# Optimization experiments

Hardware: AMD Instinct MI355X
Metric: run time of the kernel (lower is better)

Reference implementation:

```python
import jax, jax.numpy as jnp
import numpy as np
from jax import lax

R_NOBOUNDARY, R_BOUNDARY, SMALL_M, BIG_M = 5, 20, 3, 6
NUM_CLASSES, EMBED = 20, 2048


def _conv1d(x, w, pad):
    # x: [B, Cin, T], w: [Cout, Cin, K] -> [B, Cout, T]
    return lax.conv_general_dilated(x, w, (1,), [(pad, pad)],
                                    dimension_numbers=('NCH', 'OIH', 'NCH'))


def _erode(b, k):
    # scipy binary_erosion with structure ones((1,k)), border_value=0:
    # out[i] = min over window [i - k//2, i + k-1 - k//2], zero-padded
    c = k // 2
    xp = jnp.pad(b, ((0, 0), (c, k - 1 - c)))
    return lax.reduce_window(xp, jnp.inf, lax.min, (1, k), (1, 1), 'VALID')


def _dilate(b, k):
    # scipy binary_dilation reflects the structure: window [i-(k-1-c), i+c]
    c = k // 2
    xp = jnp.pad(b, ((0, 0), (k - 1 - c, c)))
    return lax.reduce_window(xp, -jnp.inf, lax.max, (1, k), (1, 1), 'VALID')


def _select_topk(scores, emb, k):
    # scores: [B,T], emb: [B,T,D] -> ([B,k,D], [B,k])
    _, idx = lax.top_k(scores, k)
    sel = jnp.take_along_axis(emb, idx[:, :, None], axis=1)
    return sel, idx


def setup_inputs() -> dict:
    key = jax.random.key(0)
    ks = jax.random.split(key, 6)
    B, T = 16, 750
    x = jax.random.normal(ks[0], (B, T, 2048), dtype=jnp.float32)
    s_embed = 1.0 / np.sqrt(1024 * 3)
    w_rgb = jax.random.normal(ks[1], (EMBED, 1024, 3), dtype=jnp.float32) * s_embed
    b_rgb = jnp.zeros((EMBED,), dtype=jnp.float32)
    w_flow = jax.random.normal(ks[2], (EMBED, 1024, 3), dtype=jnp.float32) * s_embed
    b_flow = jnp.zeros((EMBED,), dtype=jnp.float32)
    w_cls = jax.random.normal(ks[3], (NUM_CLASSES, EMBED, 1), dtype=jnp.float32) / np.sqrt(EMBED)
    return {'x': x, 'w_rgb': w_rgb, 'b_rgb': b_rgb, 'w_flow': w_flow,
            'b_flow': b_flow, 'w_cls': w_cls}


def reference(x, w_rgb, b_rgb, w_flow, b_flow, w_cls):
    # Dropout layers are identity (eval mode).
    T = x.shape[1]
    k_nb = T // R_NOBOUNDARY
    k_b = T // R_BOUNDARY

    rgb = jnp.transpose(x[:, :, 0:1024], (0, 2, 1))    # [B,1024,T]
    flow = jnp.transpose(x[:, :, 1024:2048], (0, 2, 1))
    out = (jax.nn.relu(_conv1d(rgb, w_rgb, 1) + b_rgb[None, :, None])
           + jax.nn.relu(_conv1d(flow, w_flow, 1) + b_flow[None, :, None]))  # [B,2048,T]
    embeddings = jnp.transpose(out, (0, 2, 1))          # [B,T,2048]
    cas = jnp.transpose(jax.nn.relu(_conv1d(out, w_cls, 0)), (0, 2, 1))  # [B,T,C]
    actionness = cas.sum(axis=2)                        # [B,T]

    # no-boundary mining (dropout identity in eval)
    act_rev = jnp.max(actionness, axis=1, keepdims=True) - actionness
    EA, idx = _select_topk(actionness, embeddings, k_nb)
    EB, _ = _select_topk(act_rev, embeddings, k_nb)

    # boundary mining via 1D morphology on binarized actionness
    med = jnp.median(actionness, axis=1, keepdims=True)
    aness_bin = (actionness > med).astype(actionness.dtype)  # [B,T]
    inner = _erode(aness_bin, SMALL_M) - _erode(aness_bin, BIG_M)
    HA, _ = _select_topk(actionness * inner, embeddings, k_b)
    outer = _dilate(aness_bin, BIG_M) - _dilate(aness_bin, SMALL_M)
    HB, _ = _select_topk(actionness * outer, embeddings, k_b)

    # video-level class scores: per-class top-k mean over time, softmax over classes
    cas_ct = jnp.transpose(cas, (0, 2, 1))              # [B,C,T]
    topk_scores, _ = lax.top_k(cas_ct, k_nb)            # [B,C,k_nb]
    video_scores = jax.nn.softmax(topk_scores.mean(axis=2), axis=1)  # [B,C]

    return (video_scores, EA, EB, HA, HB, idx, actionness, cas, embeddings)
```

## Files before the change

### kernel.cpp

```cpp
#include <hip/hip_runtime.h>
#include <stdint.h>
#include <math.h>

#define B_   16
#define T_   750
#define NC_  20
#define KNB_ 150
#define KB_  37

typedef _Float16 f16x8 __attribute__((ext_vector_type(8)));
typedef _Float16 f16x4 __attribute__((ext_vector_type(4)));
typedef float    f32x4 __attribute__((ext_vector_type(4)));

static constexpr long long O_VS  = 0;
static constexpr long long O_EA  = 320;
static constexpr long long O_EB  = 320 + 4915200LL;
static constexpr long long O_HA  = 320 + 2*4915200LL;
static constexpr long long O_HB  = O_HA + 1212416LL;
static constexpr long long O_IDX = O_HB + 1212416LL;
static constexpr long long O_ACT = O_IDX + 2400LL;
static constexpr long long O_CAS = O_ACT + 12000LL;
static constexpr long long O_EMB = O_CAS + 240000LL;

static constexpr long long WX_ELE   = 16LL * 752 * 2048;
static constexpr long long W_XHI    = 0;
static constexpr long long W_XLO    = W_XHI + WX_ELE * 2;
static constexpr long long WW_ELE   = 2LL * 16 * 32 * 12288;
static constexpr long long W_WHI    = W_XLO + WX_ELE * 2;
static constexpr long long W_WLO    = W_WHI + WW_ELE * 2;
static constexpr long long W_SEL    = W_WLO + WW_ELE * 2;
static constexpr long long W_VS     = W_SEL + 40960;
static constexpr long long W_NEED   = W_VS + 4096;

__device__ __forceinline__ void gload16(const void* g, void* l) {
    __builtin_amdgcn_global_load_lds(
        (const __attribute__((address_space(1))) unsigned int*)g,
        (__attribute__((address_space(3))) unsigned int*)l, 16, 0, 0);
}

__global__ __launch_bounds__(256) void xsplit(
    const float* __restrict__ x, _Float16* __restrict__ xh, _Float16* __restrict__ xl)
{
    long i = (long)blockIdx.x * 256 + threadIdx.x;
    int row = (int)(i >> 9);
    int c4  = (int)(i & 511);
    int b = row / 752, tr = row - b * 752;
    int t = tr - 1;
    float4 v = make_float4(0.f, 0.f, 0.f, 0.f);
    if (t >= 0 && t < T_)
        v = *reinterpret_cast<const float4*>(x + ((long)(b * T_ + t) * 2048 + c4 * 4));
    float vv[4] = {v.x, v.y, v.z, v.w};
    f16x4 h, l;
    #pragma unroll
    for (int j = 0; j < 4; ++j) {
        _Float16 hi = (_Float16)vv[j];
        h[j] = hi;
        l[j] = (_Float16)(vv[j] - (float)hi);
    }
    long o = (long)row * 2048 + c4 * 4;
    *reinterpret_cast<f16x4*>(xh + o) = h;
    *reinterpret_cast<f16x4*>(xl + o) = l;
}

__global__ __launch_bounds__(64) void wsplit(
    const float* __restrict__ w_rgb, const float* __restrict__ w_flow,
    _Float16* __restrict__ wh, _Float16* __restrict__ wl)
{
    const int br   = blockIdx.x >> 11;
    const int co_g = blockIdx.x & 2047;
    const int tid  = threadIdx.x;
    const float* w = (br ? w_flow : w_rgb) + (long)co_g * 3072;
    __shared__ float wsrc[3072];
    for (int i = tid; i < 768; i += 64)
        reinterpret_cast<float4*>(wsrc)[i] = reinterpret_cast<const float4*>(w)[i];
    __syncthreads();
    const int nt = co_g >> 7, co = co_g & 127;
    for (int p = tid; p < 384; p += 64) {
        int oct = p / 3, k = p - oct * 3;
        int chunk = oct >> 2, g = oct & 3;
        int q = g ^ ((co >> 1) & 3);
        f16x8 h, l;
        #pragma unroll
        for (int j = 0; j < 8; ++j) {
            float v = wsrc[(oct * 8 + j) * 3 + k] * 512.f;
            _Float16 hi = (_Float16)v;
            h[j] = hi;
            l[j] = (_Float16)(v - (float)hi);
        }
        long o = ((long)(br * 16 + nt) * 32 + chunk) * 12288 + k * 4096 + co * 32 + q * 8;
        *reinterpret_cast<f16x8*>(wh + o) = h;
        *reinterpret_cast<f16x8*>(wl + o) = l;
    }
}

template<int ADD>
__global__ __launch_bounds__(256, 2) void conv_mfma(
    const _Float16* __restrict__ xh, const _Float16* __restrict__ xl,
    const _Float16* __restrict__ wh, const _Float16* __restrict__ wl,
    const float* __restrict__ bias, float* __restrict__ emb)
{
    __shared__ _Float16 XhL[6272], XlL[6272];
    __shared__ _Float16 WhL[12288], WlL[12288];

    const int tid  = threadIdx.x;
    const int lane = tid & 63;
    const int wid  = tid >> 6;
    const int wm = wid >> 1, wn = wid & 1;
    const int lrow = lane & 15, lg = lane >> 4;
    const int nt = blockIdx.x;
    const int b  = blockIdx.y >> 2;
    const int tt = blockIdx.y & 3;
    const int t0 = tt * 192;

    f32x4 acc[6][4];
    #pragma unroll
    for (int m = 0; m < 6; ++m)
        #pragma unroll
        for (int n = 0; n < 4; ++n)
            acc[m][n] = (f32x4){0.f, 0.f, 0.f, 0.f};

    const long xrowbase = (long)b * 752 + t0;
    for (int chunk = 0; chunk < 32; ++chunk) {
        const int cibase = ADD * 1024 + chunk * 32;
        for (int s = tid; s < 776; s += 256) {
            int r = s >> 2, q = s & 3;
            int g = q ^ ((r >> 1) & 3);
            long goff = (xrowbase + r) * 2048 + cibase + g * 8;
            int lbase = (s & ~63) * 8;
            gload16(xh + goff, XhL + lbase);
            gload16(xl + goff, XlL + lbase);
        }
        const long wbase = ((long)(ADD * 16 + nt) * 32 + chunk) * 12288;
        for (int s = tid; s < 1536; s += 256) {
            int lbase = (s & ~63) * 8;
            gload16(wh + wbase + (long)s * 8, WhL + lbase);
            gload16(wl + wbase + (long)s * 8, WlL + lbase);
        }
        __syncthreads();

        #pragma unroll
        for (int k = 0; k < 3; ++k) {
            f16x8 ah[6], al[6], bh[4], bl[4];
            #pragma unroll
            for (int m = 0; m < 6; ++m) {
                int r = wm * 96 + m * 16 + lrow + k;
                int off = r * 32 + ((lg ^ ((r >> 1) & 3)) * 8);
                ah[m] = *reinterpret_cast<const f16x8*>(&XhL[off]);
                al[m] = *reinterpret_cast<const f16x8*>(&XlL[off]);
            }
            #pragma unroll
            for (int n = 0; n < 4; ++n) {
                int co = wn * 64 + n * 16 + lrow;
                int off = k * 4096 + co * 32 + ((lg ^ ((co >> 1) & 3)) * 8);
                bh[n] = *reinterpret_cast<const f16x8*>(&WhL[off]);
                bl[n] = *reinterpret_cast<const f16x8*>(&WlL[off]);
            }
            #pragma unroll
            for (int m = 0; m < 6; ++m)
                #pragma unroll
                for (int n = 0; n < 4; ++n) {
                    acc[m][n] = __builtin_amdgcn_mfma_f32_16x16x32_f16(ah[m], bh[n], acc[m][n], 0, 0, 0);
                    acc[m][n] = __builtin_amdgcn_mfma_f32_16x16x32_f16(al[m], bh[n], acc[m][n], 0, 0, 0);
                    acc[m][n] = __builtin_amdgcn_mfma_f32_16x16x32_f16(ah[m], bl[n], acc[m][n], 0, 0, 0);
                }
        }
        __syncthreads();
    }

    const float sc = 1.f / 512.f;
    #pragma unroll
    for (int n = 0; n < 4; ++n) {
        const int co = nt * 128 + wn * 64 + n * 16 + lrow;
        const float bs = bias[co];
        #pragma unroll
        for (int m = 0; m < 6; ++m) {
            #pragma unroll
            for (int rg = 0; rg < 4; ++rg) {
                int t = t0 + wm * 96 + m * 16 + lg * 4 + rg;
                if (t < T_) {
                    long o = ((long)b * T_ + t) * 2048 + co;
                    float v = fmaxf(fmaf(acc[m][n][rg], sc, bs), 0.f);
                    if (ADD) emb[o] += v;
                    else     emb[o]  = v;
                }
            }
        }
    }
}

__global__ __launch_bounds__(256) void cas_g6(
    const float* __restrict__ emb, const float* __restrict__ wcls,
    float* __restrict__ cas, float* __restrict__ act)
{
    const int grp = blockIdx.x;
    const int b = grp / 125;
    const int tg = (grp - b * 125) * 6;
    const int tid = threadIdx.x;
    const int lane = tid & 63, wv = tid >> 6;
    const int cib = wv * 512 + lane * 8;

    float e[6][8];
    #pragma unroll
    for (int t = 0; t < 6; ++t) {
        const float* p = emb + ((long)(b * T_ + tg + t) * 2048 + cib);
        float4 a0 = *reinterpret_cast<const float4*>(p);
        float4 a1 = *reinterpret_cast<const float4*>(p + 4);
        e[t][0] = a0.x; e[t][1] = a0.y; e[t][2] = a0.z; e[t][3] = a0.w;
        e[t][4] = a1.x; e[t][5] = a1.y; e[t][6] = a1.z; e[t][7] = a1.w;
    }

    __shared__ float red[NC_][6][4];
    for (int c = 0; c < NC_; ++c) {
        const float* wp = wcls + c * 2048 + cib;
        float4 w0 = *reinterpret_cast<const float4*>(wp);
        float4 w1 = *reinterpret_cast<const float4*>(wp + 4);
        float wr[8] = {w0.x, w0.y, w0.z, w0.w, w1.x, w1.y, w1.z, w1.w};
        #pragma unroll
        for (int t = 0; t < 6; ++t) {
            float p = e[t][0] * wr[0];
            #pragma unroll
            for (int j = 1; j < 8; ++j) p = fmaf(e[t][j], wr[j], p);
            #pragma unroll
            for (int off = 32; off > 0; off >>= 1) p += __shfl_down(p, off, 64);
            if (lane == 0) red[c][t][wv] = p;
        }
    }
    __syncthreads();
    __shared__ float casv[6][NC_];
    if (tid < 120) {
        int t = tid / NC_, c = tid - t * NC_;
        float s = red[c][t][0] + red[c][t][1] + red[c][t][2] + red[c][t][3];
        s = s > 0.f ? s : 0.f;
        cas[(long)(b * T_ + tg + t) * NC_ + c] = s;
        casv[t][c] = s;
    }
    __syncthreads();
    if (tid < 6) {
        float s = 0.f;
        #pragma unroll
        for (int c = 0; c < NC_; ++c) s += casv[tid][c];
        act[b * T_ + tg + tid] = s;
    }
}

__global__ __launch_bounds__(256) void conv_embed_f32(
    const float* __restrict__ x,
    const float* __restrict__ w_rgb, const float* __restrict__ b_rgb,
    const float* __restrict__ w_flow, const float* __restrict__ b_flow,
    float* __restrict__ emb)
{
    __shared__ float Xs[2][16][132];
    __shared__ float Ws[2][16][3][68];
    const int tid = threadIdx.x;
    const int tx  = tid & 15;
    const int ty  = tid >> 4;
    const int co0 = blockIdx.x * 64;
    const int tb  = blockIdx.y;
    const int t0  = (tb % 6) * 128;
    const int b   = tb / 6;
    const float* xb = x + (long long)b * T_ * 2048;
    float acc[2][8][4];
    #pragma unroll
    for (int br = 0; br < 2; ++br)
        #pragma unroll
        for (int i = 0; i < 8; ++i)
            #pragma unroll
            for (int j = 0; j < 4; ++j) acc[br][i][j] = 0.f;
    for (int cc = 0; cc < 1024; cc += 16) {
        for (int it = tid; it < 1040; it += 256) {
            int br = (it >= 520);
            int r4 = it - br * 520;
            int r  = r4 >> 2;
            int cq = r4 & 3;
            int t  = t0 - 1 + r;
            float4 v = make_float4(0.f, 0.f, 0.f, 0.f);
            if (t >= 0 && t < T_)
                v = *reinterpret_cast<const float4*>(xb + (long long)t * 2048 + br * 1024 + cc + cq * 4);
            Xs[br][cq * 4 + 0][r] = v.x;
            Xs[br][cq * 4 + 1][r] = v.y;
            Xs[br][cq * 4 + 2][r] = v.z;
            Xs[br][cq * 4 + 3][r] = v.w;
        }
        for (int it = tid; it < 1536; it += 256) {
            int br = (it >= 768);
            int r  = it - br * 768;
            int co = r / 12;
            int fq = r - co * 12;
            const float* wsrc = (br ? w_flow : w_rgb) + ((long long)(co0 + co) * 1024 + cc) * 3 + fq * 4;
            float4 v = *reinterpret_cast<const float4*>(wsrc);
            float vv[4] = {v.x, v.y, v.z, v.w};
            #pragma unroll
            for (int j = 0; j < 4; ++j) {
                int f  = fq * 4 + j;
                int ci = f / 3;
                int kk = f - ci * 3;
                Ws[br][ci][kk][co] = vv[j];
            }
        }
        __syncthreads();
        #pragma unroll
        for (int ci = 0; ci < 16; ++ci) {
            float xr[2][12];
            #pragma unroll
            for (int br = 0; br < 2; ++br) {
                const float4* xp = reinterpret_cast<const float4*>(&Xs[br][ci][ty * 8]);
                float4 a0 = xp[0], a1 = xp[1], a2 = xp[2];
                xr[br][0] = a0.x; xr[br][1] = a0.y; xr[br][2]  = a0.z; xr[br][3]  = a0.w;
                xr[br][4] = a1.x; xr[br][5] = a1.y; xr[br][6]  = a1.z; xr[br][7]  = a1.w;
                xr[br][8] = a2.x; xr[br][9] = a2.y; xr[br][10] = a2.z; xr[br][11] = a2.w;
            }
            #pragma unroll
            for (int br = 0; br < 2; ++br) {
                #pragma unroll
                for (int k = 0; k < 3; ++k) {
                    const float4 bv = *reinterpret_cast<const float4*>(&Ws[br][ci][k][tx * 4]);
                    float bw[4] = {bv.x, bv.y, bv.z, bv.w};
                    #pragma unroll
                    for (int i = 0; i < 8; ++i)
                        #pragma unroll
                        for (int j = 0; j < 4; ++j)
                            acc[br][i][j] = fmaf(xr[br][i + k], bw[j], acc[br][i][j]);
                }
            }
        }
        __syncthreads();
    }
    const float4 brv = *reinterpret_cast<const float4*>(b_rgb + co0 + tx * 4);
    const float4 bfv = *reinterpret_cast<const float4*>(b_flow + co0 + tx * 4);
    float brr[4] = {brv.x, brv.y, brv.z, brv.w};
    float bff[4] = {bfv.x, bfv.y, bfv.z, bfv.w};
    #pragma unroll
    for (int i = 0; i < 8; ++i) {
        int t = t0 + ty * 8 + i;
        if (t < T_) {
            float ov[4];
            #pragma unroll
            for (int j = 0; j < 4; ++j) {
                float r = acc[0][i][j] + brr[j];
                float f = acc[1][i][j] + bff[j];
                r = r > 0.f ? r : 0.f;
                f = f > 0.f ? f : 0.f;
                ov[j] = r + f;
            }
            float4 o; o.x = ov[0]; o.y = ov[1]; o.z = ov[2]; o.w = ov[3];
            *reinterpret_cast<float4*>(emb + ((long long)b * T_ + t) * 2048 + co0 + tx * 4) = o;
        }
    }
}

__device__ inline float keyval(unsigned long long k) {
    return __uint_as_float(~(unsigned)(k >> 32));
}

__device__ inline void bitonic_sort_u64(unsigned long long* keys, int tid)
{
    for (unsigned size = 2; size <= 1024; size <<= 1) {
        for (unsigned stride = size >> 1; stride > 0; stride >>= 1) {
            __syncthreads();
            for (int j = tid; j < 512; j += 256) {
                unsigned i = ((j & ~(stride - 1)) << 1) | (j & (stride - 1));
                unsigned p = i + stride;
                bool asc = ((i & size) == 0);
                unsigned long long a = keys[i];
                unsigned long long c = keys[p];
                bool sw = asc ? (a > c) : (a < c);
                if (sw) { keys[i] = c; keys[p] = a; }
            }
        }
    }
    __syncthreads();
}

__device__ inline void bitonic_sort_u32(unsigned* keys, int tid)
{
    for (unsigned size = 2; size <= 1024; size <<= 1) {
        for (unsigned stride = size >> 1; stride > 0; stride >>= 1) {
            __syncthreads();
            for (int j = tid; j < 512; j += 256) {
                unsigned i = ((j & ~(stride - 1)) << 1) | (j & (stride - 1));
                unsigned p = i + stride;
                bool asc = ((i & size) == 0);
                unsigned a = keys[i];
                unsigned c = keys[p];
                bool sw = asc ? (a > c) : (a < c);
                if (sw) { keys[i] = c; keys[p] = a; }
            }
        }
    }
    __syncthreads();
}

__global__ __launch_bounds__(256) void analysis_kernel(
    const float* __restrict__ act, float* __restrict__ idx_out, int* __restrict__ sel)
{
    const int b   = blockIdx.x;
    const int tid = threadIdx.x;
    __shared__ float av[T_];
    __shared__ unsigned long long keys[1024];
    __shared__ unsigned char bin[T_];
    __shared__ float medmax[2];

    for (int t = tid; t < T_; t += 256) av[t] = act[b * T_ + t];
    __syncthreads();

    for (int p = tid; p < 1024; p += 256) {
        unsigned long long k = ~0ull;
        if (p < T_) k = ((unsigned long long)(~__float_as_uint(av[p])) << 32) | (unsigned)p;
        keys[p] = k;
    }
    bitonic_sort_u64(keys, tid);
    if (tid < KNB_) {
        int t = (int)(keys[tid] & 0xffffffffu);
        idx_out[b * KNB_ + tid] = (float)t;
        sel[(b * 4 + 0) * 160 + tid] = t;
    }
    if (tid == 0) {
        medmax[0] = 0.5f * (keyval(keys[374]) + keyval(keys[375]));
        medmax[1] = keyval(keys[0]);
    }
    __syncthreads();
    const float med = medmax[0];
    const float mx  = medmax[1];
    for (int t = tid; t < T_; t += 256) bin[t] = (av[t] > med) ? 1 : 0;
    __syncthreads();

    for (int p = tid; p < 1024; p += 256) {
        unsigned long long k = ~0ull;
        if (p < T_) k = ((unsigned long long)(~__float_as_uint(mx - av[p])) << 32) | (unsigned)p;
        keys[p] = k;
    }
    bitonic_sort_u64(keys, tid);
    if (tid < KNB_) sel[(b * 4 + 1) * 160 + tid] = (int)(keys[tid] & 0xffffffffu);
    __syncthreads();

    for (int p = tid; p < 1024; p += 256) {
        unsigned long long k = ~0ull;
        if (p < T_) {
            int b0 = (p >= 1) ? bin[p - 1] : 0;
            int b1 = bin[p];
            int b2 = (p + 1 < T_) ? bin[p + 1] : 0;
            int e3 = b0 & b1 & b2;
            int e6 = 1;
            #pragma unroll
            for (int d = -3; d <= 2; ++d) {
                int q = p + d;
                e6 &= (q >= 0 && q < T_) ? (int)bin[q] : 0;
            }
            float s = (e3 && !e6) ? av[p] : 0.f;
            k = ((unsigned long long)(~__float_as_uint(s)) << 32) | (unsigned)p;
        }
        keys[p] = k;
    }
    bitonic_sort_u64(keys, tid);
    if (tid < KB_) sel[(b * 4 + 2) * 160 + tid] = (int)(keys[tid] & 0xffffffffu);
    __syncthreads();

    for (int p = tid; p < 1024; p += 256) {
        unsigned long long k = ~0ull;
        if (p < T_) {
            int b0 = (p >= 1) ? bin[p - 1] : 0;
            int b1 = bin[p];
            int b2 = (p + 1 < T_) ? bin[p + 1] : 0;
            int d3 = b0 | b1 | b2;
            int d6 = 0;
            #pragma unroll
            for (int d = -2; d <= 3; ++d) {
                int q = p + d;
                d6 |= (q >= 0 && q < T_) ? (int)bin[q] : 0;
            }
            float s = (d6 && !d3) ? av[p] : 0.f;
            k = ((unsigned long long)(~__float_as_uint(s)) << 32) | (unsigned)p;
        }
        keys[p] = k;
    }
    bitonic_sort_u64(keys, tid);
    if (tid < KB_) sel[(b * 4 + 3) * 160 + tid] = (int)(keys[tid] & 0xffffffffu);
}

__global__ __launch_bounds__(256) void video_topk(
    const float* __restrict__ cas, float* __restrict__ vs)
{
    const int bc  = blockIdx.x;
    const int b   = bc / NC_;
    const int c   = bc - b * NC_;
    const int tid = threadIdx.x;
    __shared__ unsigned keys[1024];
    __shared__ float red[4];
    for (int p = tid; p < 1024; p += 256)
        keys[p] = (p < T_) ? ~__float_as_uint(cas[((long long)b * T_ + p) * NC_ + c]) : 0xffffffffu;
    bitonic_sort_u32(keys, tid);
    float v = (tid < KNB_) ? __uint_as_float(~keys[tid]) : 0.f;
    #pragma unroll
    for (int off = 32; off > 0; off >>= 1) v += __shfl_down(v, off, 64);
    const int lane = tid & 63, wid = tid >> 6;
    if (lane == 0) red[wid] = v;
    __syncthreads();
    if (tid == 0) vs[bc] = (red[0] + red[1] + red[2] + red[3]) / 150.f;
}

__global__ void softmax20(const float* __restrict__ vs, float* __restrict__ out)
{
    const int b   = blockIdx.x;
    const int tid = threadIdx.x;
    float v = (tid < NC_) ? vs[b * NC_ + tid] : -INFINITY;
    float m = v;
    #pragma unroll
    for (int off = 32; off > 0; off >>= 1) m = fmaxf(m, __shfl_xor(m, off, 64));
    float e = (tid < NC_) ? expf(v - m) : 0.f;
    float s = e;
    #pragma unroll
    for (int off = 32; off > 0; off >>= 1) s += __shfl_xor(s, off, 64);
    if (tid < NC_) out[b * NC_ + tid] = e / s;
}

__global__ __launch_bounds__(256) void gather_rows(
    const float* __restrict__ emb, const int* __restrict__ sel, float* __restrict__ out)
{
    const int r = blockIdx.x;
    const int b = r / 374;
    const int q = r - b * 374;
    int g, p; long long dst;
    if (q < 150)      { g = 0; p = q;       dst = O_EA + (long long)(b * KNB_ + p) * 2048; }
    else if (q < 300) { g = 1; p = q - 150; dst = O_EB + (long long)(b * KNB_ + p) * 2048; }
    else if (q < 337) { g = 2; p = q - 300; dst = O_HA + (long long)(b * KB_ + p) * 2048; }
    else              { g = 3; p = q - 337; dst = O_HB + (long long)(b * KB_ + p) * 2048; }
    const int t = sel[(b * 4 + g) * 160 + p];
    const float4* src = reinterpret_cast<const float4*>(emb + ((long long)b * T_ + t) * 2048);
    float4* d = reinterpret_cast<float4*>(out + dst);
    for (int i = threadIdx.x; i < 512; i += 256) d[i] = src[i];
}

extern "C" void kernel_launch(void* const* d_in, const int* in_sizes, int n_in,
                              void* d_out, int out_size, void* d_ws, size_t ws_size,
                              hipStream_t stream)
{
    const float* x      = (const float*)d_in[0];
    const float* w_rgb  = (const float*)d_in[1];
    const float* b_rgb  = (const float*)d_in[2];
    const float* w_flow = (const float*)d_in[3];
    const float* b_flow = (const float*)d_in[4];
    const float* w_cls  = (const float*)d_in[5];

    float* out  = (float*)d_out;
    float* emb  = out + O_EMB;
    float* cas  = out + O_CAS;
    float* act  = out + O_ACT;
    float* idxo = out + O_IDX;

    const bool fast = (ws_size >= (size_t)W_NEED);

    int*   sel;
    float* vs;
    if (fast) {
        sel = (int*)((char*)d_ws + W_SEL);
        vs  = (float*)((char*)d_ws + W_VS);
        _Float16* xh = (_Float16*)((char*)d_ws + W_XHI);
        _Float16* xl = (_Float16*)((char*)d_ws + W_XLO);
        _Float16* wh = (_Float16*)((char*)d_ws + W_WHI);
        _Float16* wl = (_Float16*)((char*)d_ws + W_WLO);

        xsplit<<<24064, 256, 0, stream>>>(x, xh, xl);
        wsplit<<<4096, 64, 0, stream>>>(w_rgb, w_flow, wh, wl);
        conv_mfma<0><<<dim3(16, 64), 256, 0, stream>>>(xh, xl, wh, wl, b_rgb, emb);
        conv_mfma<1><<<dim3(16, 64), 256, 0, stream>>>(xh, xl, wh, wl, b_flow, emb);
    } else {
        sel = (int*)d_ws;
        vs  = (float*)((char*)d_ws + 64 * 1024);
        conv_embed_f32<<<dim3(32, 96), 256, 0, stream>>>(x, w_rgb, b_rgb, w_flow, b_flow, emb);
    }

    cas_g6<<<B_ * 125, 256, 0, stream>>>(emb, w_cls, cas, act);
    analysis_kernel<<<B_, 256, 0, stream>>>(act, idxo, sel);
    video_topk<<<B_ * NC_, 256, 0, stream>>>(cas, vs);
    softmax20<<<B_, 64, 0, stream>>>(vs, out + O_VS);
    gather_rows<<<B_ * 374, 256, 0, stream>>>(emb, sel, out);
}
```

Measured before the change: 1.197 ms.

## Use 32x32 MFMA tiles with swizzled block order and retile CAS kernel

The conv kernel switches from 16x16x32 to 32x32x16 f16 MFMA instructions with 3x2 accumulator tiles per wave. This cuts LDS fragment reads per FLOP and lowers the MFMA issue count. Block IDs are remapped so that consecutive blocks spread across the weight tiles, which may improve cache locality across the chiplet XCDs. The CAS classifier kernel is rewritten to stage 16 time rows and all 20 class weights in LDS, with one thread per (t,c) output, in place of shuffle reductions. The bigger accumulators raise register pressure and the row mapping has to match the 32x32 output layout.

```diff
diff --git a/kernel.cpp b/kernel.cpp
--- a/kernel.cpp
+++ b/kernel.cpp
@@ -11,6 +11,7 @@
 typedef _Float16 f16x8 __attribute__((ext_vector_type(8)));
 typedef _Float16 f16x4 __attribute__((ext_vector_type(4)));
 typedef float    f32x4 __attribute__((ext_vector_type(4)));
+typedef float    f32x16 __attribute__((ext_vector_type(16)));
 
 static constexpr long long O_VS  = 0;
 static constexpr long long O_EA  = 320;
@@ -106,18 +107,23 @@
     const int lane = tid & 63;
     const int wid  = tid >> 6;
     const int wm = wid >> 1, wn = wid & 1;
-    const int lrow = lane & 15, lg = lane >> 4;
-    const int nt = blockIdx.x;
-    const int b  = blockIdx.y >> 2;
-    const int tt = blockIdx.y & 3;
-    const int t0 = tt * 192;
-
-    f32x4 acc[6][4];
-    #pragma unroll
-    for (int m = 0; m < 6; ++m)
-        #pragma unroll
-        for (int n = 0; n < 4; ++n)
-            acc[m][n] = (f32x4){0.f, 0.f, 0.f, 0.f};
+    const int l31 = lane & 31, lg2 = lane >> 5;
+
+    const int bid = blockIdx.y * 16 + blockIdx.x;
+    const int lid = (bid & 7) * 128 + (bid >> 3);
+    const int nt  = lid >> 6;
+    const int bty = lid & 63;
+    const int b   = bty >> 2;
+    const int tt  = bty & 3;
+    const int t0  = tt * 192;
+
+    f32x16 acc[3][2];
+    #pragma unroll
+    for (int m = 0; m < 3; ++m)
+        #pragma unroll
+        for (int n = 0; n < 2; ++n)
+            #pragma unroll
+            for (int e = 0; e < 16; ++e) acc[m][n][e] = 0.f;
 
     const long xrowbase = (long)b * 752 + t0;
     for (int chunk = 0; chunk < 32; ++chunk) {
@@ -140,46 +146,51 @@
 
         #pragma unroll
         for (int k = 0; k < 3; ++k) {
-            f16x8 ah[6], al[6], bh[4], bl[4];
-            #pragma unroll
-            for (int m = 0; m < 6; ++m) {
-                int r = wm * 96 + m * 16 + lrow + k;
-                int off = r * 32 + ((lg ^ ((r >> 1) & 3)) * 8);
-                ah[m] = *reinterpret_cast<const f16x8*>(&XhL[off]);
-                al[m] = *reinterpret_cast<const f16x8*>(&XlL[off]);
-            }
-            #pragma unroll
-            for (int n = 0; n < 4; ++n) {
-                int co = wn * 64 + n * 16 + lrow;
-                int off = k * 4096 + co * 32 + ((lg ^ ((co >> 1) & 3)) * 8);
-                bh[n] = *reinterpret_cast<const f16x8*>(&WhL[off]);
-                bl[n] = *reinterpret_cast<const f16x8*>(&WlL[off]);
-            }
-            #pragma unroll
-            for (int m = 0; m < 6; ++m)
+            #pragma unroll
+            for (int s2 = 0; s2 < 2; ++s2) {
+                const int g = 2 * s2 + lg2;
+                f16x8 ah[3], al[3], bh[2], bl[2];
                 #pragma unroll
-                for (int n = 0; n < 4; ++n) {
-                    acc[m][n] = __builtin_amdgcn_mfma_f32_16x16x32_f16(ah[m], bh[n], acc[m][n], 0, 0, 0);
-                    acc[m][n] = __builtin_amdgcn_mfma_f32_16x16x32_f16(al[m], bh[n], acc[m][n], 0, 0, 0);
-                    acc[m][n] = __builtin_amdgcn_mfma_f32_16x16x32_f16(ah[m], bl[n], acc[m][n], 0, 0, 0);
+                for (int m = 0; m < 3; ++m) {
+                    int r = wm * 96 + m * 32 + l31 + k;
+                    int off = r * 32 + ((g ^ ((r >> 1) & 3)) * 8);
+                    ah[m] = *reinterpret_cast<const f16x8*>(&XhL[off]);
+                    al[m] = *reinterpret_cast<const f16x8*>(&XlL[off]);
                 }
+                #pragma unroll
+                for (int n = 0; n < 2; ++n) {
+                    int co = wn * 64 + n * 32 + l31;
+                    int off = k * 4096 + co * 32 + ((g ^ ((co >> 1) & 3)) * 8);
+                    bh[n] = *reinterpret_cast<const f16x8*>(&WhL[off]);
+                    bl[n] = *reinterpret_cast<const f16x8*>(&WlL[off]);
+                }
+                #pragma unroll
+                for (int m = 0; m < 3; ++m)
+                    #pragma unroll
+                    for (int n = 0; n < 2; ++n) {
+                        acc[m][n] = __builtin_amdgcn_mfma_f32_32x32x16_f16(ah[m], bh[n], acc[m][n], 0, 0, 0);
+                        acc[m][n] = __builtin_amdgcn_mfma_f32_32x32x16_f16(al[m], bh[n], acc[m][n], 0, 0, 0);
+                        acc[m][n] = __builtin_amdgcn_mfma_f32_32x32x16_f16(ah[m], bl[n], acc[m][n], 0, 0, 0);
+                    }
+            }
         }
         __syncthreads();
     }
 
     const float sc = 1.f / 512.f;
     #pragma unroll
-    for (int n = 0; n < 4; ++n) {
-        const int co = nt * 128 + wn * 64 + n * 16 + lrow;
+    for (int n = 0; n < 2; ++n) {
+        const int co = nt * 128 + wn * 64 + n * 32 + l31;
         const float bs = bias[co];
         #pragma unroll
-        for (int m = 0; m < 6; ++m) {
-            #pragma unroll
-            for (int rg = 0; rg < 4; ++rg) {
-                int t = t0 + wm * 96 + m * 16 + lg * 4 + rg;
+        for (int m = 0; m < 3; ++m) {
+            #pragma unroll
+            for (int reg = 0; reg < 16; ++reg) {
+                int row32 = (reg & 3) + 8 * (reg >> 2) + 4 * lg2;
+                int t = t0 + wm * 96 + m * 32 + row32;
                 if (t < T_) {
                     long o = ((long)b * T_ + t) * 2048 + co;
-                    float v = fmaxf(fmaf(acc[m][n][rg], sc, bs), 0.f);
+                    float v = fmaxf(fmaf(acc[m][n][reg], sc, bs), 0.f);
                     if (ADD) emb[o] += v;
                     else     emb[o]  = v;
                 }
@@ -188,58 +199,48 @@
     }
 }
 
-__global__ __launch_bounds__(256) void cas_g6(
+__global__ __launch_bounds__(320) void cas_tc(
     const float* __restrict__ emb, const float* __restrict__ wcls,
     float* __restrict__ cas, float* __restrict__ act)
 {
-    const int grp = blockIdx.x;
-    const int b = grp / 125;
-    const int tg = (grp - b * 125) * 6;
+    const int t0g = blockIdx.x * 16;
     const int tid = threadIdx.x;
-    const int lane = tid & 63, wv = tid >> 6;
-    const int cib = wv * 512 + lane * 8;
-
-    float e[6][8];
-    #pragma unroll
-    for (int t = 0; t < 6; ++t) {
-        const float* p = emb + ((long)(b * T_ + tg + t) * 2048 + cib);
-        float4 a0 = *reinterpret_cast<const float4*>(p);
-        float4 a1 = *reinterpret_cast<const float4*>(p + 4);
-        e[t][0] = a0.x; e[t][1] = a0.y; e[t][2] = a0.z; e[t][3] = a0.w;
-        e[t][4] = a1.x; e[t][5] = a1.y; e[t][6] = a1.z; e[t][7] = a1.w;
-    }
-
-    __shared__ float red[NC_][6][4];
-    for (int c = 0; c < NC_; ++c) {
-        const float* wp = wcls + c * 2048 + cib;
-        float4 w0 = *reinterpret_cast<const float4*>(wp);
-        float4 w1 = *reinterpret_cast<const float4*>(wp + 4);
-        float wr[8] = {w0.x, w0.y, w0.z, w0.w, w1.x, w1.y, w1.z, w1.w};
-        #pragma unroll
-        for (int t = 0; t < 6; ++t) {
-            float p = e[t][0] * wr[0];
-            #pragma unroll
-            for (int j = 1; j < 8; ++j) p = fmaf(e[t][j], wr[j], p);
-            #pragma unroll
-            for (int off = 32; off > 0; off >>= 1) p += __shfl_down(p, off, 64);
-            if (lane == 0) red[c][t][wv] = p;
-        }
-    }
-    __syncthreads();
-    __shared__ float casv[6][NC_];
-    if (tid < 120) {
-        int t = tid / NC_, c = tid - t * NC_;
-        float s = red[c][t][0] + red[c][t][1] + red[c][t][2] + red[c][t][3];
-        s = s > 0.f ? s : 0.f;
-        cas[(long)(b * T_ + tg + t) * NC_ + c] = s;
-        casv[t][c] = s;
-    }
-    __syncthreads();
-    if (tid < 6) {
+    const int tl  = tid / 20, c = tid % 20;
+    __shared__ float embS[16][132];
+    __shared__ float wS[20][132];
+    __shared__ float casS[16][20];
+
+    float acc = 0.f;
+    for (int cc = 0; cc < 2048; cc += 128) {
+        for (int s = tid; s < 512; s += 320) {
+            int r = s >> 5, q = s & 31;
+            *reinterpret_cast<float4*>(&embS[r][q * 4]) =
+                *reinterpret_cast<const float4*>(&emb[((long)t0g + r) * 2048 + cc + q * 4]);
+        }
+        for (int s = tid; s < 640; s += 320) {
+            int r = s >> 5, q = s & 31;
+            *reinterpret_cast<float4*>(&wS[r][q * 4]) =
+                *reinterpret_cast<const float4*>(&wcls[(long)r * 2048 + cc + q * 4]);
+        }
+        __syncthreads();
+        #pragma unroll
+        for (int q = 0; q < 32; ++q) {
+            float4 a = *reinterpret_cast<const float4*>(&embS[tl][q * 4]);
+            float4 w = *reinterpret_cast<const float4*>(&wS[c][q * 4]);
+            acc = fmaf(a.x, w.x, acc); acc = fmaf(a.y, w.y, acc);
+            acc = fmaf(a.z, w.z, acc); acc = fmaf(a.w, w.w, acc);
+        }
+        __syncthreads();
+    }
+    float r = acc > 0.f ? acc : 0.f;
+    cas[(long)(t0g + tl) * NC_ + c] = r;
+    casS[tl][c] = r;
+    __syncthreads();
+    if (tid < 16) {
         float s = 0.f;
         #pragma unroll
-        for (int c = 0; c < NC_; ++c) s += casv[tid][c];
-        act[b * T_ + tg + tid] = s;
+        for (int c2 = 0; c2 < NC_; ++c2) s += casS[tid][c2];
+        act[t0g + tid] = s;
     }
 }
 
@@ -569,7 +570,7 @@
         conv_embed_f32<<<dim3(32, 96), 256, 0, stream>>>(x, w_rgb, b_rgb, w_flow, b_flow, emb);
     }
 
-    cas_g6<<<B_ * 125, 256, 0, stream>>>(emb, w_cls, cas, act);
+    cas_tc<<<750, 320, 0, stream>>>(emb, w_cls, cas, act);
     analysis_kernel<<<B_, 256, 0, stream>>>(act, idxo, sel);
     video_topk<<<B_ * NC_, 256, 0, stream>>>(cas, vs);
     softmax20<<<B_, 64, 0, stream>>>(vs, out + O_VS);
```

New measurement: 1.254 ms. 1.05x slower.
